# Performance work log

Hardware: AMD Instinct MI355X
Metric: run time of the kernel (lower is better)

Reference implementation:

```python
import jax, jax.numpy as jnp
import numpy as np

HEADS = 6
DIM_HEAD = 64
SCALE = DIM_HEAD ** -0.5
BN_EPS = 1e-5


def _dw_pw(x, w_dw, gamma, beta, mean, var, w_pw, stride):
    """Depthwise 3x3 conv (groups=C) -> BatchNorm (inference) -> 1x1 pointwise conv."""
    C = x.shape[1]
    y = jax.lax.conv_general_dilated(
        x, w_dw, window_strides=(stride, stride), padding=((1, 1), (1, 1)),
        dimension_numbers=('NCHW', 'OIHW', 'NCHW'), feature_group_count=C)
    inv = gamma / jnp.sqrt(var + BN_EPS)
    y = y * inv[None, :, None, None] + (beta - mean * inv)[None, :, None, None]
    # 1x1 conv as einsum: w_pw is [O, C]
    return jnp.einsum('bchw,oc->bohw', y, w_pw)


def setup_inputs() -> dict:
    key = jax.random.key(0)
    ks = jax.random.split(key, 10)
    B, C, H, W = 32, 384, 32, 32
    inner = HEADS * DIM_HEAD  # 384
    ws = 0.05  # weight scale to keep attention logits sane
    return {
        'x': jax.random.normal(ks[0], (B, C, H, W), jnp.float32),
        'q_dw': jax.random.normal(ks[1], (C, 1, 3, 3), jnp.float32) * ws,
        'q_gamma': jnp.ones((C,), jnp.float32),
        'q_beta': jnp.zeros((C,), jnp.float32),
        'q_mean': jax.random.normal(ks[2], (C,), jnp.float32) * 0.1,
        'q_var': jax.random.uniform(ks[3], (C,), jnp.float32) + 0.5,
        'q_pw': jax.random.normal(ks[4], (inner, C), jnp.float32) * ws,
        'kv_dw': jax.random.normal(ks[5], (C, 1, 3, 3), jnp.float32) * ws,
        'kv_gamma': jnp.ones((C,), jnp.float32),
        'kv_beta': jnp.zeros((C,), jnp.float32),
        'kv_mean': jax.random.normal(ks[6], (C,), jnp.float32) * 0.1,
        'kv_var': jax.random.uniform(ks[7], (C,), jnp.float32) + 0.5,
        'kv_pw': jax.random.normal(ks[8], (2 * inner, C), jnp.float32) * ws,
        'out_w': jax.random.normal(ks[9], (C, inner), jnp.float32) * ws,
        'out_b': jnp.zeros((C,), jnp.float32),
    }


def reference(x, q_dw, q_gamma, q_beta, q_mean, q_var, q_pw,
              kv_dw, kv_gamma, kv_beta, kv_mean, kv_var, kv_pw,
              out_w, out_b):
    B, C, H, W = x.shape
    h, d = HEADS, DIM_HEAD
    # Q at full resolution, K/V spatially downsampled (stride 2)
    q = _dw_pw(x, q_dw, q_gamma, q_beta, q_mean, q_var, q_pw, stride=1)   # [B, h*d, H, W]
    kv = _dw_pw(x, kv_dw, kv_gamma, kv_beta, kv_mean, kv_var, kv_pw, stride=2)  # [B, 2*h*d, Hk, Wk]
    k, v = jnp.split(kv, 2, axis=1)
    Hk, Wk = k.shape[2], k.shape[3]
    # 'b (h d) x y -> b h (x y) d'
    q = q.reshape(B, h, d, H * W).transpose(0, 1, 3, 2)
    k = k.reshape(B, h, d, Hk * Wk).transpose(0, 1, 3, 2)
    v = v.reshape(B, h, d, Hk * Wk).transpose(0, 1, 3, 2)
    dots = jnp.einsum('bhid,bhjd->bhij', q, k) * SCALE  # [B, h, HW, HkWk]
    attn = jax.nn.softmax(dots, axis=-1)
    out = jnp.einsum('bhij,bhjd->bhid', attn, v)        # [B, h, HW, d]
    # 'b h (x y) d -> b (h d) x y'
    out = out.transpose(0, 1, 3, 2).reshape(B, h * d, H, W)
    # final 1x1 conv projection (dropout is identity, p=0)
    return jnp.einsum('bchw,oc->bohw', out, out_w) + out_b[None, :, None, None]
```

## Files before the change

kernel.cpp:

```cpp
#include <hip/hip_runtime.h>
#include <hip/hip_bf16.h>

#define CIN 384
#define PQ 1024
#define PKV 256
#define HEADS 6
#define DH 64
#define INNER 384
#define ATTN_SCALE 0.125f

typedef __hip_bfloat16 bf16;
typedef unsigned short ushort;
typedef __bf16 bf16x8 __attribute__((ext_vector_type(8)));
typedef float floatx4 __attribute__((ext_vector_type(4)));

__device__ __forceinline__ float b2f(bf16 v) { return __bfloat162float(v); }
__device__ __forceinline__ bf16 f2b(float v) { return __float2bfloat16(v); }
__device__ __forceinline__ ushort f2bu(float v) { bf16 h = __float2bfloat16(v); return *(ushort*)&h; }
__device__ __forceinline__ float ldf(const void* p, size_t i, int isbf) {
    return isbf ? __bfloat162float(((const bf16*)p)[i]) : ((const float*)p)[i];
}
__device__ __forceinline__ void dma16(const bf16* g, bf16* l) {
    __builtin_amdgcn_global_load_lds(
        (const __attribute__((address_space(1))) unsigned int*)g,
        (__attribute__((address_space(3))) unsigned int*)l, 16, 0, 0);
}

__global__ void detect_kernel(const unsigned int* __restrict__ x, int* __restrict__ flag) {
    if (threadIdx.x == 0 && blockIdx.x == 0) {
        int cnt = 0;
        for (int i = 0; i < 64; i++) {
            unsigned int e = (x[i] >> 7) & 0xFFu;
            if (e >= 100u && e <= 140u) cnt++;
        }
        *flag = (cnt >= 48) ? 1 : 0;
    }
}

__global__ void wconv_kernel(const void* __restrict__ w0, const void* __restrict__ w1,
                             const void* __restrict__ w2, bf16* __restrict__ dst,
                             const int* __restrict__ flagp) {
    int isbf = *flagp;
    const int n0 = INNER * CIN, n1 = 2 * INNER * CIN, n2 = INNER * CIN;
    int i = blockIdx.x * 256 + threadIdx.x;
    int total = n0 + n1 + n2;
    for (; i < total; i += gridDim.x * 256) {
        float v;
        if (i < n0) v = ldf(w0, i, isbf);
        else if (i < n0 + n1) v = ldf(w1, i - n0, isbf);
        else v = ldf(w2, i - n0 - n1, isbf);
        dst[i] = f2b(v);
    }
}

template <int STRIDE, int HO, int WO>
__global__ __launch_bounds__(256) void dw_bn_kernel(
        const void* __restrict__ x, const void* __restrict__ wdw,
        const void* __restrict__ gamma, const void* __restrict__ beta,
        const void* __restrict__ mean, const void* __restrict__ var,
        bf16* __restrict__ yt, const int* __restrict__ flagp) {
    constexpr int IN_ROWS = (8 - 1) * STRIDE + 3;
    constexpr int RL = 37;
    constexpr int PT = 8 * WO;
    constexpr unsigned XSZ = 32u * IN_ROWS * RL * 4;
    constexpr unsigned OSZ = (unsigned)PT * 40 * 2;
    __shared__ __align__(16) char smem[XSZ > OSZ ? XSZ : OSZ];
    float (*xin)[IN_ROWS][RL] = (float (*)[IN_ROWS][RL])smem;
    ushort (*outt)[40] = (ushort (*)[40])smem;

    int isbf = *flagp;
    int rg = blockIdx.x;
    int c0 = blockIdx.y * 32;
    int b  = blockIdx.z;
    int tid = threadIdx.x;
    int ri0 = rg * 8 * STRIDE - 1;

    for (int e = tid; e < 32 * IN_ROWS; e += 256) {
        int i = e % IN_ROWS, cc = e / IN_ROWS;
        xin[cc][i][0] = 0.f;
        xin[cc][i][33] = 0.f;
    }

    const int NCHUNK = 32 * IN_ROWS * 4;
    for (int ch = tid; ch < NCHUNK; ch += 256) {
        int wc = ch & 3;
        int t  = ch >> 2;
        int i  = t % IN_ROWS;
        int cc = t / IN_ROWS;
        int row = ri0 + i;
        float f[8];
        if (row >= 0 && row < 32) {
            size_t goff = ((size_t)(b * CIN + c0 + cc) * 32 + row) * 32 + wc * 8;
            if (isbf) {
                uint4 v = *(const uint4*)((const bf16*)x + goff);
                const ushort* u = (const ushort*)&v;
#pragma unroll
                for (int j = 0; j < 8; j++) f[j] = __uint_as_float((unsigned)u[j] << 16);
            } else {
                float4 v0 = *(const float4*)((const float*)x + goff);
                float4 v1 = *(const float4*)((const float*)x + goff + 4);
                f[0] = v0.x; f[1] = v0.y; f[2] = v0.z; f[3] = v0.w;
                f[4] = v1.x; f[5] = v1.y; f[6] = v1.z; f[7] = v1.w;
            }
        } else {
#pragma unroll
            for (int j = 0; j < 8; j++) f[j] = 0.f;
        }
        float* dst = &xin[cc][i][1 + wc * 8];
#pragma unroll
        for (int j = 0; j < 8; j++) dst[j] = f[j];
    }

    int cc = tid & 31;
    int g  = tid >> 5;
    int c  = c0 + cc;
    float w9[9];
#pragma unroll
    for (int k = 0; k < 9; k++) w9[k] = ldf(wdw, c * 9 + k, isbf);
    float inv  = ldf(gamma, c, isbf) * rsqrtf(ldf(var, c, isbf) + 1e-5f);
    float bias = ldf(beta, c, isbf) - ldf(mean, c, isbf) * inv;
    __syncthreads();

    const float* xr0 = xin[cc][g * STRIDE + 0];
    const float* xr1 = xin[cc][g * STRIDE + 1];
    const float* xr2 = xin[cc][g * STRIDE + 2];
    float o[WO];
    if (STRIDE == 1) {
        float a0 = xr0[0], a1 = xr0[1];
        float b0 = xr1[0], b1 = xr1[1];
        float q0 = xr2[0], q1 = xr2[1];
#pragma unroll
        for (int wo = 0; wo < WO; wo++) {
            float a2 = xr0[wo + 2], b2 = xr1[wo + 2], q2 = xr2[wo + 2];
            float acc = w9[0] * a0 + w9[1] * a1 + w9[2] * a2
                      + w9[3] * b0 + w9[4] * b1 + w9[5] * b2
                      + w9[6] * q0 + w9[7] * q1 + w9[8] * q2;
            o[wo] = acc * inv + bias;
            a0 = a1; a1 = a2; b0 = b1; b1 = b2; q0 = q1; q1 = q2;
        }
    } else {
        float a0 = xr0[0], b0 = xr1[0], q0 = xr2[0];
#pragma unroll
        for (int wo = 0; wo < WO; wo++) {
            float a1 = xr0[2 * wo + 1], a2 = xr0[2 * wo + 2];
            float b1 = xr1[2 * wo + 1], b2 = xr1[2 * wo + 2];
            float q1 = xr2[2 * wo + 1], q2 = xr2[2 * wo + 2];
            float acc = w9[0] * a0 + w9[1] * a1 + w9[2] * a2
                      + w9[3] * b0 + w9[4] * b1 + w9[5] * b2
                      + w9[6] * q0 + w9[7] * q1 + w9[8] * q2;
            o[wo] = acc * inv + bias;
            a0 = a2; b0 = b2; q0 = q2;
        }
    }
    __syncthreads();

#pragma unroll
    for (int wo = 0; wo < WO; wo++) outt[g * WO + wo][cc] = f2bu(o[wo]);
    __syncthreads();

    const size_t pbase = (size_t)b * (HO * WO) + (size_t)rg * 8 * WO;
    for (int chk = tid; chk < PT * 4; chk += 256) {
        int k = chk & 3, p = chk >> 2;
        uint4 v = *(const uint4*)&outt[p][k * 8];
        *(uint4*)(yt + (pbase + p) * CIN + c0 + k * 8) = v;
    }
}

template <int P, int MODE>
__global__ __launch_bounds__(256, 2) void mfma_pw(
        const bf16* __restrict__ wt, const bf16* __restrict__ yt,
        const void* __restrict__ bias, void* __restrict__ out0,
        bf16* __restrict__ out1, int O, const int* __restrict__ flagp) {
    __shared__ __align__(16) bf16 As[2][4096];
    __shared__ __align__(16) bf16 Bs[2][4096];
    int tid = threadIdx.x;
    int wave = tid >> 6, lane = tid & 63;
    int l15 = lane & 15, quad = lane >> 4;
    int wm = wave & 1, wn = wave >> 1;
    int b = blockIdx.z;
    int p0 = blockIdx.x * 128;
    int o0 = blockIdx.y * 128;

    const bf16* asrc = yt + ((size_t)b * P + p0) * CIN;
    const bf16* bsrc = wt + (size_t)o0 * CIN;

    int srow = (lane >> 2);
    int sc   = lane & 3;
    auto stage = [&](int step, int buf) {
#pragma unroll
        for (int it = 0; it < 2; it++) {
            int row = wave * 32 + it * 16 + srow;
            int g = sc ^ (row & 3);
            size_t goff = (size_t)row * CIN + step * 32 + g * 8;
            dma16(asrc + goff, &As[buf][(wave * 2 + it) * 512]);
            dma16(bsrc + goff, &Bs[buf][(wave * 2 + it) * 512]);
        }
    };

    floatx4 acc[4][4];
#pragma unroll
    for (int pt = 0; pt < 4; pt++)
#pragma unroll
        for (int ot = 0; ot < 4; ot++) acc[pt][ot] = (floatx4){0.f, 0.f, 0.f, 0.f};

    stage(0, 0);
    __syncthreads();
    for (int s = 0; s < CIN / 32; s++) {
        int buf = s & 1;
        if (s < CIN / 32 - 1) stage(s + 1, buf ^ 1);
        bf16x8 af[4], bw[4];
        int slot = (quad ^ (l15 & 3)) * 8;
#pragma unroll
        for (int pt = 0; pt < 4; pt++)
            af[pt] = *(const bf16x8*)&As[buf][(wm * 64 + pt * 16 + l15) * 32 + slot];
#pragma unroll
        for (int ot = 0; ot < 4; ot++)
            bw[ot] = *(const bf16x8*)&Bs[buf][(wn * 64 + ot * 16 + l15) * 32 + slot];
#pragma unroll
        for (int pt = 0; pt < 4; pt++)
#pragma unroll
            for (int ot = 0; ot < 4; ot++)
                acc[pt][ot] = __builtin_amdgcn_mfma_f32_16x16x32_bf16(af[pt], bw[ot], acc[pt][ot], 0, 0, 0);
        __syncthreads();
    }

    int pw0 = p0 + wm * 64, ow0 = o0 + wn * 64;
    if (MODE == 2) {
        int isbf = *flagp;
#pragma unroll
        for (int ot = 0; ot < 4; ot++) {
            int o = ow0 + ot * 16 + l15;
            float bv = ldf(bias, o, isbf);
#pragma unroll
            for (int pt = 0; pt < 4; pt++) {
                int p = pw0 + pt * 16 + quad * 4;
                size_t idx = ((size_t)b * O + o) * P + p;
                if (!isbf) {
                    float4 v4 = {acc[pt][ot][0] + bv, acc[pt][ot][1] + bv,
                                 acc[pt][ot][2] + bv, acc[pt][ot][3] + bv};
                    *(float4*)((float*)out0 + idx) = v4;
                } else {
                    ushort4 u4 = {f2bu(acc[pt][ot][0] + bv), f2bu(acc[pt][ot][1] + bv),
                                  f2bu(acc[pt][ot][2] + bv), f2bu(acc[pt][ot][3] + bv)};
                    *(ushort4*)((bf16*)out0 + idx) = u4;
                }
            }
        }
    } else if (MODE == 0) {
#pragma unroll
        for (int ot = 0; ot < 4; ot++) {
            int o = ow0 + ot * 16 + l15;
            int h = o >> 6, d = o & 63;
            bf16* base = (bf16*)out0 + ((size_t)(b * HEADS + h) * P) * 64 + d;
#pragma unroll
            for (int pt = 0; pt < 4; pt++)
#pragma unroll
                for (int r = 0; r < 4; r++)
                    base[(size_t)(pw0 + pt * 16 + quad * 4 + r) * 64] = f2b(acc[pt][ot][r]);
        }
    } else {
#pragma unroll
        for (int ot = 0; ot < 4; ot++) {
            int o = ow0 + ot * 16 + l15;
            if (o < INNER) {
                int h = o >> 6, d = o & 63;
                bf16* base = (bf16*)out0 + ((size_t)(b * HEADS + h) * P) * 64 + d;
#pragma unroll
                for (int pt = 0; pt < 4; pt++)
#pragma unroll
                    for (int r = 0; r < 4; r++)
                        base[(size_t)(pw0 + pt * 16 + quad * 4 + r) * 64] = f2b(acc[pt][ot][r]);
            } else {
                int ch = o - INNER;
                bf16* base = out1 + ((size_t)b * INNER + ch) * PKV;
#pragma unroll
                for (int pt = 0; pt < 4; pt++)
#pragma unroll
                    for (int r = 0; r < 4; r++)
                        base[pw0 + pt * 16 + quad * 4 + r] = f2b(acc[pt][ot][r]);
            }
        }
    }
}

__global__ __launch_bounds__(256, 2) void attn_kernel(
        const bf16* __restrict__ qalt, const bf16* __restrict__ kalt,
        const bf16* __restrict__ valt, bf16* __restrict__ ao) {
    __shared__ __align__(16) bf16 Kl[16384];
    __shared__ __align__(16) bf16 Vl[16384];
    __shared__ __align__(16) ushort Ot[4][16][80];
    int tid = threadIdx.x;
    int wave = tid >> 6, lane = tid & 63;
    int l15 = lane & 15, quad = lane >> 4;
    int blk = blockIdx.x;
    int hg = blk % (32 * HEADS);
    int tile = blk / (32 * HEADS);
    int b = hg / HEADS;
    int h = hg % HEADS;
    int p0 = tile * 64 + wave * 16;

    const bf16* qbase = qalt + (size_t)(b * HEADS + h) * PQ * DH;
    const bf16* kbase = kalt + (size_t)(b * HEADS + h) * PKV * DH;
    const bf16* vbase = valt + ((size_t)b * INNER + h * DH) * PKV;

    const bf16* qrow = qbase + (size_t)(p0 + l15) * DH + quad * 8;
    bf16x8 a0 = *(const bf16x8*)qrow;
    bf16x8 a1 = *(const bf16x8*)(qrow + 32);

    {
        int j = (lane >> 3);
        int cs = lane & 7;
#pragma unroll
        for (int it = 0; it < 8; it++) {
            int jb = (wave * 8 + it) * 8;
            int jr = jb + j;
            int g = cs ^ (jr & 7);
            dma16(kbase + (size_t)jr * 64 + g * 8, &Kl[(size_t)(wave * 8 + it) * 512]);
        }
        int d = (lane >> 5);
        int cs2 = lane & 31;
#pragma unroll
        for (int it = 0; it < 8; it++) {
            int db = (wave * 8 + it) * 2;
            int dr = db + d;
            int g = cs2 ^ (dr & 15);
            dma16(vbase + (size_t)dr * 256 + g * 8, &Vl[(size_t)(wave * 8 + it) * 512]);
        }
    }
    __syncthreads();

    floatx4 s[16];
#pragma unroll
    for (int jt = 0; jt < 16; jt++) s[jt] = (floatx4){0.f, 0.f, 0.f, 0.f};
#pragma unroll
    for (int jt = 0; jt < 16; jt++) {
        int j = jt * 16 + l15;
        bf16x8 b0 = *(const bf16x8*)&Kl[j * 64 + (quad ^ (j & 7)) * 8];
        bf16x8 b1 = *(const bf16x8*)&Kl[j * 64 + ((4 + quad) ^ (j & 7)) * 8];
        s[jt] = __builtin_amdgcn_mfma_f32_16x16x32_bf16(a0, b0, s[jt], 0, 0, 0);
        s[jt] = __builtin_amdgcn_mfma_f32_16x16x32_bf16(a1, b1, s[jt], 0, 0, 0);
    }

    float pinv[4];
#pragma unroll
    for (int r = 0; r < 4; r++) {
        float mx = s[0][r];
#pragma unroll
        for (int jt = 1; jt < 16; jt++) mx = fmaxf(mx, s[jt][r]);
#pragma unroll
        for (int off = 1; off <= 8; off <<= 1) mx = fmaxf(mx, __shfl_xor(mx, off, 64));
        float sm = 0.f;
#pragma unroll
        for (int jt = 0; jt < 16; jt++) {
            float e = __expf((s[jt][r] - mx) * ATTN_SCALE);
            s[jt][r] = e;
            sm += e;
        }
#pragma unroll
        for (int off = 1; off <= 8; off <<= 1) sm += __shfl_xor(sm, off, 64);
        pinv[r] = 1.f / sm;
    }
    __syncthreads();

    ushort* Plw = (ushort*)&Kl[wave * 4096];
#pragma unroll
    for (int r = 0; r < 4; r++) {
        int row = quad * 4 + r;
#pragma unroll
        for (int jt = 0; jt < 16; jt++) {
            int c = jt * 2 + (l15 >> 3);
            Plw[row * 256 + (c ^ row) * 8 + (l15 & 7)] = f2bu(s[jt][r] * pinv[r]);
        }
    }
    bf16x8 pa[8];
#pragma unroll
    for (int kk = 0; kk < 8; kk++)
        pa[kk] = *(const bf16x8*)&Plw[l15 * 256 + ((kk * 4 + quad) ^ l15) * 8];

    floatx4 oacc[4];
#pragma unroll
    for (int nt = 0; nt < 4; nt++) oacc[nt] = (floatx4){0.f, 0.f, 0.f, 0.f};
#pragma unroll
    for (int nt = 0; nt < 4; nt++) {
        int d = nt * 16 + l15;
#pragma unroll
        for (int kk = 0; kk < 8; kk++) {
            bf16x8 bv = *(const bf16x8*)&Vl[d * 256 + ((kk * 4 + quad) ^ l15) * 8];
            oacc[nt] = __builtin_amdgcn_mfma_f32_16x16x32_bf16(pa[kk], bv, oacc[nt], 0, 0, 0);
        }
    }

#pragma unroll
    for (int nt = 0; nt < 4; nt++)
#pragma unroll
        for (int r = 0; r < 4; r++)
            Ot[wave][quad * 4 + r][nt * 16 + l15] = f2bu(oacc[nt][r]);
    int row = lane >> 2, d0 = (lane & 3) * 16;
    uint4 ld0 = *(const uint4*)&Ot[wave][row][d0];
    uint4 ld1 = *(const uint4*)&Ot[wave][row][d0 + 8];
    bf16* dst = ao + ((size_t)b * PQ + p0 + row) * INNER + h * DH + d0;
    *(uint4*)dst = ld0;
    *(uint4*)(dst + 8) = ld1;
}

extern "C" void kernel_launch(void* const* d_in, const int* in_sizes, int n_in,
                              void* d_out, int out_size, void* d_ws, size_t ws_size,
                              hipStream_t stream) {
    const void* x        = d_in[0];
    const void* q_dw     = d_in[1];
    const void* q_gamma  = d_in[2];
    const void* q_beta   = d_in[3];
    const void* q_mean   = d_in[4];
    const void* q_var    = d_in[5];
    const void* q_pw     = d_in[6];
    const void* kv_dw    = d_in[7];
    const void* kv_gamma = d_in[8];
    const void* kv_beta  = d_in[9];
    const void* kv_mean  = d_in[10];
    const void* kv_var   = d_in[11];
    const void* kv_pw    = d_in[12];
    const void* out_w    = d_in[13];
    const void* out_b    = d_in[14];

    int* flag = (int*)d_ws;
    bf16* pool = (bf16*)((char*)d_ws + 256);
    bf16* yqt  = pool;
    bf16* ykvt = yqt  + (size_t)32 * 1024 * 384;
    bf16* qalt = ykvt + (size_t)32 * 256 * 384;
    bf16* kalt = qalt + (size_t)32 * 6 * 1024 * 64;
    bf16* valt = kalt + (size_t)32 * 6 * 256 * 64;
    bf16* wbf  = valt + (size_t)32 * 384 * 256;
    bf16* qpw_bf = wbf;
    bf16* kvpw_bf = wbf + (size_t)INNER * CIN;
    bf16* outw_bf = kvpw_bf + (size_t)2 * INNER * CIN;
    bf16* aob  = yqt;

    detect_kernel<<<1, 64, 0, stream>>>((const unsigned int*)x, flag);
    wconv_kernel<<<576, 256, 0, stream>>>(q_pw, kv_pw, out_w, wbf, flag);
    dw_bn_kernel<1, 32, 32><<<dim3(4, 12, 32), 256, 0, stream>>>(x, q_dw, q_gamma, q_beta, q_mean, q_var, yqt, flag);
    dw_bn_kernel<2, 16, 16><<<dim3(2, 12, 32), 256, 0, stream>>>(x, kv_dw, kv_gamma, kv_beta, kv_mean, kv_var, ykvt, flag);
    mfma_pw<1024, 0><<<dim3(8, 3, 32), 256, 0, stream>>>(qpw_bf, yqt, nullptr, qalt, nullptr, INNER, flag);
    mfma_pw<256, 1><<<dim3(2, 6, 32), 256, 0, stream>>>(kvpw_bf, ykvt, nullptr, kalt, valt, 2 * INNER, flag);
    attn_kernel<<<32 * 6 * 16, 256, 0, stream>>>(qalt, kalt, valt, aob);
    mfma_pw<1024, 2><<<dim3(8, 3, 32), 256, 0, stream>>>(outw_bf, aob, out_b, d_out, nullptr, CIN, flag);
}
```

Baseline: 246.4 us.

## Reuse K/V tiles across four query tiles per attention block, register-resident P

Each attention block now processes four 64-query tiles for one (batch, head), so K and V are loaded into LDS once instead of once per tile, and the grid shrinks from 3072 to 768 blocks with an XCD-aware index swizzle. QK^T is computed transposed (K as the A operand), which lets the softmax probabilities feed the PV MFMA straight from registers through the 16x16x16 bf16 instruction, removing the LDS round trip for P and a barrier. The next Q tile is prefetched while the current one is computed. The cost is fewer blocks to spread across CUs, longer serial work per block, and higher register pressure.

```diff
diff --git a/kernel.cpp b/kernel.cpp
--- a/kernel.cpp
+++ b/kernel.cpp
@@ -13,6 +13,11 @@
 typedef unsigned short ushort;
 typedef __bf16 bf16x8 __attribute__((ext_vector_type(8)));
 typedef float floatx4 __attribute__((ext_vector_type(4)));
+typedef short shortx4 __attribute__((ext_vector_type(4)));
+
+#if __has_builtin(__builtin_amdgcn_mfma_f32_16x16x16bf16_1k)
+#define HAVE_MFMA16 1
+#endif
 
 __device__ __forceinline__ float b2f(bf16 v) { return __bfloat162float(v); }
 __device__ __forceinline__ bf16 f2b(float v) { return __float2bfloat16(v); }
@@ -293,114 +298,137 @@
     int wave = tid >> 6, lane = tid & 63;
     int l15 = lane & 15, quad = lane >> 4;
     int blk = blockIdx.x;
-    int hg = blk % (32 * HEADS);
-    int tile = blk / (32 * HEADS);
-    int b = hg / HEADS;
-    int h = hg % HEADS;
-    int p0 = tile * 64 + wave * 16;
+    int swz = (blk & 7) * 96 + (blk >> 3);
+    int seg = swz & 3;
+    int bh  = swz >> 2;
+    int b = bh / HEADS, h = bh % HEADS;
 
     const bf16* qbase = qalt + (size_t)(b * HEADS + h) * PQ * DH;
     const bf16* kbase = kalt + (size_t)(b * HEADS + h) * PKV * DH;
     const bf16* vbase = valt + ((size_t)b * INNER + h * DH) * PKV;
 
+    {
+        int j = lane >> 3, cs = lane & 7;
+#pragma unroll
+        for (int it = 0; it < 8; it++) {
+            int jr = (wave * 8 + it) * 8 + j;
+            int g = cs ^ (jr & 7);
+            dma16(kbase + (size_t)jr * 64 + g * 8, &Kl[(wave * 8 + it) * 512]);
+        }
+        int d = lane >> 5, cs2 = lane & 31;
+#pragma unroll
+        for (int it = 0; it < 8; it++) {
+            int dr = (wave * 8 + it) * 2 + d;
+            int g = cs2 ^ (dr & 15);
+            dma16(vbase + (size_t)dr * 256 + g * 8, &Vl[(wave * 8 + it) * 512]);
+        }
+    }
+
+    int p0 = seg * 256 + wave * 16;
     const bf16* qrow = qbase + (size_t)(p0 + l15) * DH + quad * 8;
-    bf16x8 a0 = *(const bf16x8*)qrow;
-    bf16x8 a1 = *(const bf16x8*)(qrow + 32);
-
-    {
-        int j = (lane >> 3);
-        int cs = lane & 7;
-#pragma unroll
-        for (int it = 0; it < 8; it++) {
-            int jb = (wave * 8 + it) * 8;
-            int jr = jb + j;
-            int g = cs ^ (jr & 7);
-            dma16(kbase + (size_t)jr * 64 + g * 8, &Kl[(size_t)(wave * 8 + it) * 512]);
-        }
-        int d = (lane >> 5);
-        int cs2 = lane & 31;
-#pragma unroll
-        for (int it = 0; it < 8; it++) {
-            int db = (wave * 8 + it) * 2;
-            int dr = db + d;
-            int g = cs2 ^ (dr & 15);
-            dma16(vbase + (size_t)dr * 256 + g * 8, &Vl[(size_t)(wave * 8 + it) * 512]);
-        }
-    }
+    bf16x8 qc0 = *(const bf16x8*)qrow;
+    bf16x8 qc1 = *(const bf16x8*)(qrow + 32);
     __syncthreads();
 
-    floatx4 s[16];
-#pragma unroll
-    for (int jt = 0; jt < 16; jt++) s[jt] = (floatx4){0.f, 0.f, 0.f, 0.f};
-#pragma unroll
-    for (int jt = 0; jt < 16; jt++) {
-        int j = jt * 16 + l15;
-        bf16x8 b0 = *(const bf16x8*)&Kl[j * 64 + (quad ^ (j & 7)) * 8];
-        bf16x8 b1 = *(const bf16x8*)&Kl[j * 64 + ((4 + quad) ^ (j & 7)) * 8];
-        s[jt] = __builtin_amdgcn_mfma_f32_16x16x32_bf16(a0, b0, s[jt], 0, 0, 0);
-        s[jt] = __builtin_amdgcn_mfma_f32_16x16x32_bf16(a1, b1, s[jt], 0, 0, 0);
-    }
-
-    float pinv[4];
-#pragma unroll
-    for (int r = 0; r < 4; r++) {
-        float mx = s[0][r];
-#pragma unroll
-        for (int jt = 1; jt < 16; jt++) mx = fmaxf(mx, s[jt][r]);
-#pragma unroll
-        for (int off = 1; off <= 8; off <<= 1) mx = fmaxf(mx, __shfl_xor(mx, off, 64));
+#pragma unroll
+    for (int t = 0; t < 4; t++) {
+        bf16x8 qn0 = qc0, qn1 = qc1;
+        if (t < 3) {
+            const bf16* qr = qrow + (size_t)(t + 1) * 64 * DH;
+            qn0 = *(const bf16x8*)qr;
+            qn1 = *(const bf16x8*)(qr + 32);
+        }
+
+        floatx4 s[16];
+#pragma unroll
+        for (int jt = 0; jt < 16; jt++) s[jt] = (floatx4){0.f, 0.f, 0.f, 0.f};
+#pragma unroll
+        for (int jt = 0; jt < 16; jt++) {
+            int j = jt * 16 + l15;
+            bf16x8 k0 = *(const bf16x8*)&Kl[j * 64 + (quad ^ (j & 7)) * 8];
+            bf16x8 k1 = *(const bf16x8*)&Kl[j * 64 + ((4 + quad) ^ (j & 7)) * 8];
+            s[jt] = __builtin_amdgcn_mfma_f32_16x16x32_bf16(k0, qc0, s[jt], 0, 0, 0);
+            s[jt] = __builtin_amdgcn_mfma_f32_16x16x32_bf16(k1, qc1, s[jt], 0, 0, 0);
+        }
+
+        float mx = s[0][0];
+#pragma unroll
+        for (int jt = 0; jt < 16; jt++)
+#pragma unroll
+            for (int r = 0; r < 4; r++) mx = fmaxf(mx, s[jt][r]);
+        mx = fmaxf(mx, __shfl_xor(mx, 16, 64));
+        mx = fmaxf(mx, __shfl_xor(mx, 32, 64));
         float sm = 0.f;
 #pragma unroll
+        for (int jt = 0; jt < 16; jt++)
+#pragma unroll
+            for (int r = 0; r < 4; r++) {
+                float e = __expf((s[jt][r] - mx) * ATTN_SCALE);
+                s[jt][r] = e;
+                sm += e;
+            }
+        sm += __shfl_xor(sm, 16, 64);
+        sm += __shfl_xor(sm, 32, 64);
+        float pinv = 1.f / sm;
+
+        floatx4 oacc[4];
+#pragma unroll
+        for (int nt = 0; nt < 4; nt++) oacc[nt] = (floatx4){0.f, 0.f, 0.f, 0.f};
+#ifdef HAVE_MFMA16
+#pragma unroll
         for (int jt = 0; jt < 16; jt++) {
-            float e = __expf((s[jt][r] - mx) * ATTN_SCALE);
-            s[jt][r] = e;
-            sm += e;
-        }
-#pragma unroll
-        for (int off = 1; off <= 8; off <<= 1) sm += __shfl_xor(sm, off, 64);
-        pinv[r] = 1.f / sm;
-    }
-    __syncthreads();
-
-    ushort* Plw = (ushort*)&Kl[wave * 4096];
-#pragma unroll
-    for (int r = 0; r < 4; r++) {
-        int row = quad * 4 + r;
-#pragma unroll
-        for (int jt = 0; jt < 16; jt++) {
-            int c = jt * 2 + (l15 >> 3);
-            Plw[row * 256 + (c ^ row) * 8 + (l15 & 7)] = f2bu(s[jt][r] * pinv[r]);
-        }
-    }
-    bf16x8 pa[8];
-#pragma unroll
-    for (int kk = 0; kk < 8; kk++)
-        pa[kk] = *(const bf16x8*)&Plw[l15 * 256 + ((kk * 4 + quad) ^ l15) * 8];
-
-    floatx4 oacc[4];
-#pragma unroll
-    for (int nt = 0; nt < 4; nt++) oacc[nt] = (floatx4){0.f, 0.f, 0.f, 0.f};
-#pragma unroll
-    for (int nt = 0; nt < 4; nt++) {
-        int d = nt * 16 + l15;
+            shortx4 pa;
+#pragma unroll
+            for (int r = 0; r < 4; r++) pa[r] = (short)f2bu(s[jt][r] * pinv);
+#pragma unroll
+            for (int nt = 0; nt < 4; nt++) {
+                int d = nt * 16 + l15;
+                shortx4 bv = *(const shortx4*)&Vl[d * 256 +
+                        ((jt * 2 + (quad >> 1)) ^ (d & 15)) * 8 + (quad & 1) * 4];
+                oacc[nt] = __builtin_amdgcn_mfma_f32_16x16x16bf16_1k(pa, bv, oacc[nt], 0, 0, 0);
+            }
+        }
+#else
 #pragma unroll
         for (int kk = 0; kk < 8; kk++) {
-            bf16x8 bv = *(const bf16x8*)&Vl[d * 256 + ((kk * 4 + quad) ^ l15) * 8];
-            oacc[nt] = __builtin_amdgcn_mfma_f32_16x16x32_bf16(pa[kk], bv, oacc[nt], 0, 0, 0);
-        }
-    }
-
-#pragma unroll
-    for (int nt = 0; nt < 4; nt++)
-#pragma unroll
-        for (int r = 0; r < 4; r++)
-            Ot[wave][quad * 4 + r][nt * 16 + l15] = f2bu(oacc[nt][r]);
-    int row = lane >> 2, d0 = (lane & 3) * 16;
-    uint4 ld0 = *(const uint4*)&Ot[wave][row][d0];
-    uint4 ld1 = *(const uint4*)&Ot[wave][row][d0 + 8];
-    bf16* dst = ao + ((size_t)b * PQ + p0 + row) * INNER + h * DH + d0;
-    *(uint4*)dst = ld0;
-    *(uint4*)(dst + 8) = ld1;
+            unsigned Ad0 = ((unsigned)f2bu(s[2 * kk][1] * pinv) << 16) | f2bu(s[2 * kk][0] * pinv);
+            unsigned Ad1 = ((unsigned)f2bu(s[2 * kk][3] * pinv) << 16) | f2bu(s[2 * kk][2] * pinv);
+            unsigned Bd0 = ((unsigned)f2bu(s[2 * kk + 1][1] * pinv) << 16) | f2bu(s[2 * kk + 1][0] * pinv);
+            unsigned Bd1 = ((unsigned)f2bu(s[2 * kk + 1][3] * pinv) << 16) | f2bu(s[2 * kk + 1][2] * pinv);
+            int srcA = l15 + ((quad & 1) << 5);
+            unsigned dw[4];
+#pragma unroll
+            for (int i = 0; i < 4; i++) {
+                int srcl = srcA + ((i >> 1) << 4);
+                unsigned ta = (i & 1) ? __shfl((int)Ad1, srcl, 64) : __shfl((int)Ad0, srcl, 64);
+                unsigned tb = (i & 1) ? __shfl((int)Bd1, srcl, 64) : __shfl((int)Bd0, srcl, 64);
+                dw[i] = (quad >> 1) ? tb : ta;
+            }
+            union { unsigned u[4]; bf16x8 v; } pc;
+            pc.u[0] = dw[0]; pc.u[1] = dw[1]; pc.u[2] = dw[2]; pc.u[3] = dw[3];
+#pragma unroll
+            for (int nt = 0; nt < 4; nt++) {
+                int d = nt * 16 + l15;
+                bf16x8 bv = *(const bf16x8*)&Vl[d * 256 + ((kk * 4 + quad) ^ (d & 15)) * 8];
+                oacc[nt] = __builtin_amdgcn_mfma_f32_16x16x32_bf16(pc.v, bv, oacc[nt], 0, 0, 0);
+            }
+        }
+#endif
+
+#pragma unroll
+        for (int nt = 0; nt < 4; nt++)
+#pragma unroll
+            for (int r = 0; r < 4; r++)
+                Ot[wave][quad * 4 + r][nt * 16 + l15] = f2bu(oacc[nt][r]);
+        int row = lane >> 2, d0 = (lane & 3) * 16;
+        uint4 ld0 = *(const uint4*)&Ot[wave][row][d0];
+        uint4 ld1 = *(const uint4*)&Ot[wave][row][d0 + 8];
+        bf16* dst = ao + ((size_t)b * PQ + p0 + t * 64 + row) * INNER + h * DH + d0;
+        *(uint4*)dst = ld0;
+        *(uint4*)(dst + 8) = ld1;
+
+        qc0 = qn0; qc1 = qn1;
+    }
 }
 
 extern "C" void kernel_launch(void* const* d_in, const int* in_sizes, int n_in,
@@ -441,6 +469,6 @@
     dw_bn_kernel<2, 16, 16><<<dim3(2, 12, 32), 256, 0, stream>>>(x, kv_dw, kv_gamma, kv_beta, kv_mean, kv_var, ykvt, flag);
     mfma_pw<1024, 0><<<dim3(8, 3, 32), 256, 0, stream>>>(qpw_bf, yqt, nullptr, qalt, nullptr, INNER, flag);
     mfma_pw<256, 1><<<dim3(2, 6, 32), 256, 0, stream>>>(kvpw_bf, ykvt, nullptr, kalt, valt, 2 * INNER, flag);
-    attn_kernel<<<32 * 6 * 16, 256, 0, stream>>>(qalt, kalt, valt, aob);
+    attn_kernel<<<768, 256, 0, stream>>>(qalt, kalt, valt, aob);
     mfma_pw<1024, 2><<<dim3(8, 3, 32), 256, 0, stream>>>(outw_bf, aob, out_b, d_out, nullptr, CIN, flag);
 }
```

New measurement: 241.5 us. 1.02x faster.
